# Performance work log

Measured on AMD Instinct MI355X. Metric: run time of the kernel, lower is better.

The kernel has to match this reference:

```python
import jax, jax.numpy as jnp
import numpy as np

DIM = 1024
HEADS = 16
DIM_HEAD = DIM // HEADS
SCALE = DIM_HEAD ** -0.5
LN_EPS = 1e-5


def setup_inputs() -> dict:
    key = jax.random.key(0)
    ks = jax.random.split(key, 10)
    b, n, m = 2, 2048, 2048
    s = 0.02
    return {
        "x": jax.random.normal(ks[0], (b, n, DIM), jnp.float32),
        "context": jax.random.normal(ks[1], (b, m, DIM), jnp.float32),
        "alibi": jax.random.normal(ks[2], (HEADS, n, m), jnp.float32),
        "Wq": jax.random.normal(ks[3], (DIM, DIM), jnp.float32) * s,
        "Wk": jax.random.normal(ks[4], (DIM, DIM), jnp.float32) * s,
        "Wv": jax.random.normal(ks[5], (DIM, DIM), jnp.float32) * s,
        "Wo": jax.random.normal(ks[6], (DIM, DIM), jnp.float32) * s,
        "bo": jnp.zeros((DIM,), jnp.float32),
        "ln_w": jnp.ones((DIM,), jnp.float32),
        "ln_b": jnp.zeros((DIM,), jnp.float32),
    }


def _layernorm(t, w, b):
    mu = jnp.mean(t, axis=-1, keepdims=True)
    var = jnp.var(t, axis=-1, keepdims=True)
    return (t - mu) * jax.lax.rsqrt(var + LN_EPS) * w + b


def reference(x, context, alibi, Wq, Wk, Wv, Wo, bo, ln_w, ln_b):
    xn = _layernorm(x, ln_w, ln_b)
    cn = _layernorm(context, ln_w, ln_b)
    # torch Linear: y = x @ W.T
    q = xn @ Wq.T
    k = cn @ Wk.T
    v = cn @ Wv.T
    b, n, _ = q.shape
    m = k.shape[1]
    # b n (h d) -> b h n d
    q = q.reshape(b, n, HEADS, DIM_HEAD).transpose(0, 2, 1, 3)
    k = k.reshape(b, m, HEADS, DIM_HEAD).transpose(0, 2, 1, 3)
    v = v.reshape(b, m, HEADS, DIM_HEAD).transpose(0, 2, 1, 3)
    scores = jnp.einsum("bhid,bhjd->bhij", q, k) * SCALE + alibi
    attn = jax.nn.softmax(scores, axis=-1)
    out = jnp.einsum("bhij,bhjd->bhid", attn, v)
    out = out.transpose(0, 2, 1, 3).reshape(b, n, HEADS * DIM_HEAD)
    return out @ Wo.T + bo
```

## Files before the change

kernel.cpp:

```cpp
#include <hip/hip_runtime.h>
#include <stdint.h>

#define DIM 1024
#define HEADS 16
#define DHEAD 64
#define LN_EPS 1e-5f
#define SCALE 0.125f
#define LOG2E 1.44269504089f
#define SMAX 4.0f

typedef _Float16 h8 __attribute__((ext_vector_type(8)));
typedef _Float16 h4 __attribute__((ext_vector_type(4)));
typedef _Float16 h2 __attribute__((ext_vector_type(2)));
typedef float f32x4 __attribute__((ext_vector_type(4)));

typedef __attribute__((address_space(1))) void* as1p;
typedef __attribute__((address_space(3))) void* as3p;

__device__ __forceinline__ void gl_lds16(const void* g, void* l) {
  __builtin_amdgcn_global_load_lds((as1p)g, (as3p)l, 16, 0, 0);
}

__device__ __forceinline__ float wave_sum(float v) {
#pragma unroll
  for (int o = 32; o > 0; o >>= 1) v += __shfl_xor(v, o, 64);
  return v;
}

__global__ __launch_bounds__(256) void cast4_kernel(const float* __restrict__ W0,
                                                    const float* __restrict__ W1,
                                                    const float* __restrict__ W2,
                                                    const float* __restrict__ W3,
                                                    _Float16* __restrict__ dst) {
  int gi = blockIdx.x * 256 + threadIdx.x;
  int wsel = gi >> 18;
  int li = gi & 0x3FFFF;
  const float* s = W0;
  if (wsel == 1) s = W1;
  else if (wsel == 2) s = W2;
  else if (wsel == 3) s = W3;
  float4 f = ((const float4*)s)[li];
  h4 o;
  o[0] = (_Float16)f.x; o[1] = (_Float16)f.y;
  o[2] = (_Float16)f.z; o[3] = (_Float16)f.w;
  ((h4*)dst)[gi] = o;
}

__global__ __launch_bounds__(256) void ln_f16(const float* __restrict__ x,
                                              const float* __restrict__ context,
                                              _Float16* __restrict__ out,
                                              const float* __restrict__ w,
                                              const float* __restrict__ b) {
  int row = blockIdx.x;
  const float* src = (row < 4096) ? x : context;
  int srow = row & 4095;
  const float4* rp = (const float4*)(src + (size_t)srow * DIM);
  float4 v = rp[threadIdx.x];
  float s = v.x + v.y + v.z + v.w;
  float ss = fmaf(v.x, v.x, fmaf(v.y, v.y, fmaf(v.z, v.z, v.w * v.w)));
  s = wave_sum(s);
  ss = wave_sum(ss);
  __shared__ float red[8];
  int wid = threadIdx.x >> 6, lane = threadIdx.x & 63;
  if (lane == 0) { red[wid] = s; red[4 + wid] = ss; }
  __syncthreads();
  s = red[0] + red[1] + red[2] + red[3];
  ss = red[4] + red[5] + red[6] + red[7];
  float mu = s * (1.0f / DIM);
  float var = ss * (1.0f / DIM) - mu * mu;
  float inv = rsqrtf(var + LN_EPS);
  float4 wv = ((const float4*)w)[threadIdx.x];
  float4 bv = ((const float4*)b)[threadIdx.x];
  h4 o;
  o[0] = (_Float16)((v.x - mu) * inv * wv.x + bv.x);
  o[1] = (_Float16)((v.y - mu) * inv * wv.y + bv.y);
  o[2] = (_Float16)((v.z - mu) * inv * wv.z + bv.z);
  o[3] = (_Float16)((v.w - mu) * inv * wv.w + bv.w);
  *(h4*)(out + (size_t)row * DIM + 4 * threadIdx.x) = o;
}

template <int OUT_MODE>
__device__ __forceinline__ void gemm_core128(const _Float16* __restrict__ A,
                                             const _Float16* __restrict__ W,
                                             void* __restrict__ C,
                                             const float* __restrict__ bias,
                                             int rowBase, int colBase) {
  __shared__ _Float16 As[128 * 64];
  __shared__ _Float16 Bs[128 * 64];
  int tid = threadIdx.x;
  int w = tid >> 6, lane = tid & 63;
  int quad = lane >> 4, l15 = lane & 15;
  int wr = w >> 1, wc = w & 1;
  f32x4 acc[4][4] = {};

  for (int k0 = 0; k0 < DIM; k0 += 64) {
#pragma unroll
    for (int l = 0; l < 4; l++) {
      int id = l * 256 + tid;
      int row = id & 127, c = id >> 7;
      gl_lds16(A + (size_t)(rowBase + row) * DIM + k0 + c * 8,
               &As[(l * 256 + w * 64) * 8]);
    }
#pragma unroll
    for (int l = 0; l < 4; l++) {
      int id = l * 256 + tid;
      int row = id & 127, c = id >> 7;
      gl_lds16(W + (size_t)(colBase + row) * DIM + k0 + c * 8,
               &Bs[(l * 256 + w * 64) * 8]);
    }
    __syncthreads();

    h8 af[2][4], bf[2][4];
#pragma unroll
    for (int ks = 0; ks < 2; ks++) {
#pragma unroll
      for (int mg = 0; mg < 4; mg++)
        af[ks][mg] = *(const h8*)&As[((ks * 4 + quad) * 128 + wr * 64 + mg * 16 + l15) * 8];
#pragma unroll
      for (int ng = 0; ng < 4; ng++)
        bf[ks][ng] = *(const h8*)&Bs[((ks * 4 + quad) * 128 + wc * 64 + ng * 16 + l15) * 8];
    }
#pragma unroll
    for (int mg = 0; mg < 4; mg++)
#pragma unroll
      for (int ng = 0; ng < 4; ng++)
#pragma unroll
        for (int ks = 0; ks < 2; ks++)
          acc[mg][ng] = __builtin_amdgcn_mfma_f32_16x16x32_f16(af[ks][mg], bf[ks][ng], acc[mg][ng], 0, 0, 0);
    __syncthreads();
  }

#pragma unroll
  for (int mg = 0; mg < 4; mg++)
#pragma unroll
    for (int ng = 0; ng < 4; ng++) {
      int ccol = colBase + wc * 64 + ng * 16 + l15;
      float bv = (OUT_MODE == 1) ? bias[ccol] : 0.f;
#pragma unroll
      for (int r = 0; r < 4; r++) {
        int crow = rowBase + wr * 64 + mg * 16 + quad * 4 + r;
        if (OUT_MODE == 0)
          ((_Float16*)C)[(size_t)crow * DIM + ccol] = (_Float16)acc[mg][ng][r];
        else
          ((float*)C)[(size_t)crow * DIM + ccol] = acc[mg][ng][r] + bv;
      }
    }
}

__global__ __launch_bounds__(256) void gemm_out(const _Float16* __restrict__ A,
                                                const _Float16* __restrict__ W,
                                                float* __restrict__ C,
                                                const float* __restrict__ bias) {
  gemm_core128<1>(A, W, C, bias, blockIdx.y * 128, blockIdx.x * 128);
}


#define G256_BAR __builtin_amdgcn_s_barrier()
#define G256_WV4 asm volatile("s_waitcnt vmcnt(4)" ::: "memory")
#define G256_WL0 asm volatile("s_waitcnt lgkmcnt(0)" ::: "memory")

#define G256_STG(matIsB, b, h, t)                                              \
  do {                                                                         \
    const _Float16* _src = (matIsB) ? Wbase : Abase;                           \
    int _slot = (matIsB) * 4 + (b) * 2 + (h);                                  \
    int _k0 = ((t) & 15) * 64;                                                 \
    gl_lds16(_src + (size_t)(h) * 128 * DIM + _k0 + sc * 8,                    \
             &lds[_slot * 8192 + (sc * 128 + rh64) * 8]);                      \
    gl_lds16(_src + (size_t)(h) * 128 * DIM + _k0 + (sc + 4) * 8,              \
             &lds[_slot * 8192 + ((sc + 4) * 128 + rh64) * 8]);                \
  } while (0)

#define G256_LDA(dst, b, mh)                                                   \
  do {                                                                         \
    _Pragma("unroll") for (int ks = 0; ks < 2; ks++)                           \
        _Pragma("unroll") for (int m = 0; m < 4; m++)                          \
            dst[ks][m] = *(const h8*)&lds[((b) * 2 + wr) * 8192 +              \
                ((ks * 4 + quad) * 128 + (mh) * 64 + m * 16 + l15) * 8];       \
  } while (0)

#define G256_LDB(dst, b, nh)                                                   \
  do {                                                                         \
    _Pragma("unroll") for (int ks = 0; ks < 2; ks++)                           \
        _Pragma("unroll") for (int n = 0; n < 2; n++)                          \
            dst[ks][n] = *(const h8*)&lds[(4 + (b) * 2 + (wc >> 1)) * 8192 +   \
                ((ks * 4 + quad) * 128 + (wc & 1) * 64 +                       \
                 ((nh) * 2 + n) * 16 + l15) * 8];                              \
  } while (0)

#define G256_MM(a_, b_, mh, nh)                                                \
  do {                                                                         \
    __builtin_amdgcn_s_setprio(1);                                             \
    _Pragma("unroll") for (int m = 0; m < 4; m++)                              \
        _Pragma("unroll") for (int n = 0; n < 2; n++)                          \
            _Pragma("unroll") for (int ks = 0; ks < 2; ks++)                   \
                acc[(mh) * 4 + m][(nh) * 2 + n] =                              \
                    __builtin_amdgcn_mfma_f32_16x16x32_f16(                    \
                        a_[ks][m], b_[ks][n], acc[(mh) * 4 + m][(nh) * 2 + n], \
                        0, 0, 0);                                              \
    __builtin_amdgcn_s_setprio(0);                                             \
  } while (0)

__global__ __launch_bounds__(512, 2) void gemm_qkv256(
    const _Float16* __restrict__ xnh, const _Float16* __restrict__ cnh,
    const _Float16* __restrict__ wq, const _Float16* __restrict__ wk,
    const _Float16* __restrict__ wv, _Float16* __restrict__ qo,
    _Float16* __restrict__ ko, _Float16* __restrict__ vo) {
  int z = blockIdx.z;
  const _Float16* A = (z == 0) ? xnh : cnh;
  const _Float16* W = (z == 0) ? wq : (z == 1) ? wk : wv;
  _Float16* C = (z == 0) ? qo : (z == 1) ? ko : vo;
  int rowBase = blockIdx.y * 256, colBase = blockIdx.x * 256;

  __shared__ __align__(16) _Float16 lds[8 * 8192];
  int tid = threadIdx.x;
  int w = tid >> 6, lane = tid & 63;
  int quad = lane >> 4, l15 = lane & 15;
  int wr = w >> 2, wc = w & 3;

  int sc = w >> 1;
  int rh64 = (w & 1) * 64;
  const _Float16* Abase = A + (size_t)(rowBase + rh64 + lane) * DIM;
  const _Float16* Wbase = W + (size_t)(colBase + rh64 + lane) * DIM;

  f32x4 acc[8][4] = {};
  h8 af[2][4], bf0[2][2], bf1[2][2];

  G256_STG(1, 0, 0, 0);
  G256_STG(1, 0, 1, 0);
  G256_STG(0, 0, 0, 0);
  G256_STG(0, 0, 1, 0);
  G256_STG(1, 1, 0, 1);
  G256_STG(1, 1, 1, 1);
  G256_WV4;
  G256_BAR;

  for (int i = 0; i < 8; i++) {
    int t1 = 2 * i + 1, t2 = 2 * i + 2, t3 = 2 * i + 3;
    G256_LDA(af, 0, 0);
    G256_LDB(bf0, 0, 0);
    G256_STG(0, 1, 0, t1);
    G256_BAR; G256_WL0;
    G256_MM(af, bf0, 0, 0);
    G256_BAR;
    G256_LDB(bf1, 0, 1);
    G256_STG(0, 1, 1, t1);
    G256_BAR; G256_WL0;
    G256_MM(af, bf1, 0, 1);
    G256_BAR;
    G256_LDA(af, 0, 1);
    G256_STG(1, 0, 0, t2);
    G256_BAR; G256_WL0;
    G256_MM(af, bf1, 1, 1);
    G256_BAR;
    G256_STG(1, 0, 1, t2);
    G256_BAR;
    G256_MM(af, bf0, 1, 0);
    G256_WV4;
    G256_BAR;
    G256_LDA(af, 1, 0);
    G256_LDB(bf0, 1, 0);
    G256_STG(0, 0, 0, t2);
    G256_BAR; G256_WL0;
    G256_MM(af, bf0, 0, 0);
    G256_BAR;
    G256_LDB(bf1, 1, 1);
    G256_STG(0, 0, 1, t2);
    G256_BAR; G256_WL0;
    G256_MM(af, bf1, 0, 1);
    G256_BAR;
    G256_LDA(af, 1, 1);
    G256_STG(1, 1, 0, t3);
    G256_BAR; G256_WL0;
    G256_MM(af, bf1, 1, 1);
    G256_BAR;
    G256_STG(1, 1, 1, t3);
    G256_BAR;
    G256_MM(af, bf0, 1, 0);
    G256_WV4;
    G256_BAR;
  }

#pragma unroll
  for (int m8 = 0; m8 < 8; m8++)
#pragma unroll
    for (int n4 = 0; n4 < 4; n4++) {
      int ccol = colBase + wc * 64 + n4 * 16 + l15;
#pragma unroll
      for (int r = 0; r < 4; r++) {
        int crow = rowBase + wr * 128 + m8 * 16 + quad * 4 + r;
        C[(size_t)crow * DIM + ccol] = (_Float16)acc[m8][n4][r];
      }
    }
}

__global__ __launch_bounds__(512) void attn_mfma(const _Float16* __restrict__ q,
                                                 const _Float16* __restrict__ k,
                                                 const _Float16* __restrict__ v,
                                                 const float* __restrict__ alibi,
                                                 _Float16* __restrict__ out) {
  __shared__ _Float16 Ks[2][2][64 * 64];
  __shared__ _Float16 Vt[2][2][64][72];
  __shared__ _Float16 Ps[2][8][16][72];

  int tid = threadIdx.x;
  int w = tid >> 6, lane = tid & 63;
  int quad = lane >> 4, l15 = lane & 15;
  int qbase = blockIdx.x * 128;
  int h = blockIdx.y;

  const _Float16 qs = (_Float16)(SCALE * LOG2E);
  h8 qf[2][2];
#pragma unroll
  for (int bi = 0; bi < 2; bi++) {
    const _Float16* qp = q + (size_t)(bi * 2048 + qbase + w * 16 + l15) * DIM + h * DHEAD;
    qf[bi][0] = *(const h8*)(qp + quad * 8) * qs;
    qf[bi][1] = *(const h8*)(qp + 32 + quad * 8) * qs;
  }

  h8 ones;
#pragma unroll
  for (int i = 0; i < 8; i++) ones[i] = (_Float16)1.0f;

  const float NEG_M2 = -SMAX * LOG2E;
  f32x4 l_acc[2] = {};
  f32x4 o_acc[2][4] = {};

  const float* arow_base = alibi + (size_t)h * 2048 * 2048 +
                           (size_t)(qbase + w * 16 + quad * 4) * 2048;

  int vbi = tid >> 8, vtt = tid & 255, vm = vtt & 15, vdg = vtt >> 4;

  float av[4][4];
#pragma unroll
  for (int r = 0; r < 4; r++)
#pragma unroll
    for (int ng = 0; ng < 4; ng++)
      av[r][ng] = arow_base[(size_t)r * 2048 + ng * 16 + l15];

#pragma unroll
  for (int l = 0; l < 2; l++) {
    int idx = w * 2 + l, sbi = idx >> 3, c = idx & 7;
    gl_lds16(k + (size_t)(sbi * 2048 + lane) * DIM + h * DHEAD + c * 8,
             &Ks[sbi][0][(c * 64) * 8]);
  }
  {
    const _Float16* vs = v + (size_t)(vbi * 2048 + vm) * DIM + h * DHEAD + vdg * 4;
    h4 a0 = *(const h4*)(vs);
    h4 a1 = *(const h4*)(vs + 16 * DIM);
    h4 a2 = *(const h4*)(vs + 32 * DIM);
    h4 a3 = *(const h4*)(vs + 48 * DIM);
#pragma unroll
    for (int i = 0; i < 4; i++) {
      h4 pk; pk[0] = a0[i]; pk[1] = a1[i]; pk[2] = a2[i]; pk[3] = a3[i];
      *(h4*)&Vt[vbi][0][vdg * 4 + i][4 * vm] = pk;
    }
  }
  __syncthreads();

  for (int t = 0; t < 32; t++) {
    int buf = t & 1;
    float avn[4][4];
    if (t + 1 < 32) {
      int kb1 = (t + 1) * 64;
#pragma unroll
      for (int l = 0; l < 2; l++) {
        int idx = w * 2 + l, sbi = idx >> 3, c = idx & 7;
        gl_lds16(k + (size_t)(sbi * 2048 + kb1 + lane) * DIM + h * DHEAD + c * 8,
                 &Ks[sbi][buf ^ 1][(c * 64) * 8]);
      }
      const _Float16* vs = v + (size_t)(vbi * 2048 + kb1 + vm) * DIM + h * DHEAD + vdg * 4;
      h4 a0 = *(const h4*)(vs);
      h4 a1 = *(const h4*)(vs + 16 * DIM);
      h4 a2 = *(const h4*)(vs + 32 * DIM);
      h4 a3 = *(const h4*)(vs + 48 * DIM);
#pragma unroll
      for (int i = 0; i < 4; i++) {
        h4 pk; pk[0] = a0[i]; pk[1] = a1[i]; pk[2] = a2[i]; pk[3] = a3[i];
        *(h4*)&Vt[vbi][buf ^ 1][vdg * 4 + i][4 * vm] = pk;
      }
#pragma unroll
      for (int r = 0; r < 4; r++)
#pragma unroll
        for (int ng = 0; ng < 4; ng++)
          avn[r][ng] = arow_base[(size_t)r * 2048 + kb1 + ng * 16 + l15];
    }

#pragma unroll
    for (int bi = 0; bi < 2; bi++) {
      f32x4 s_acc[4];
#pragma unroll
      for (int ng = 0; ng < 4; ng++) {
        s_acc[ng][0] = NEG_M2; s_acc[ng][1] = NEG_M2;
        s_acc[ng][2] = NEG_M2; s_acc[ng][3] = NEG_M2;
      }
#pragma unroll
      for (int ng = 0; ng < 4; ng++)
#pragma unroll
        for (int ks = 0; ks < 2; ks++) {
          h8 bfr = *(const h8*)&Ks[bi][buf][((ks * 4 + quad) * 64 + ng * 16 + l15) * 8];
          s_acc[ng] = __builtin_amdgcn_mfma_f32_16x16x32_f16(qf[bi][ks], bfr, s_acc[ng], 0, 0, 0);
        }

#pragma unroll
      for (int r = 0; r < 4; r++) {
        h4 pk;
#pragma unroll
        for (int ng = 0; ng < 4; ng++)
          pk[ng] = (_Float16)exp2f(fmaf(av[r][ng], LOG2E, s_acc[ng][r]));
        *(h4*)&Ps[bi][w][quad * 4 + r][4 * l15] = pk;
      }

      h8 pf[2];
      pf[0] = *(const h8*)&Ps[bi][w][l15][quad * 8];
      pf[1] = *(const h8*)&Ps[bi][w][l15][32 + quad * 8];
      l_acc[bi] = __builtin_amdgcn_mfma_f32_16x16x32_f16(pf[0], ones, l_acc[bi], 0, 0, 0);
      l_acc[bi] = __builtin_amdgcn_mfma_f32_16x16x32_f16(pf[1], ones, l_acc[bi], 0, 0, 0);
#pragma unroll
      for (int ngd = 0; ngd < 4; ngd++)
#pragma unroll
        for (int ks = 0; ks < 2; ks++) {
          h8 vf = *(const h8*)&Vt[bi][buf][ngd * 16 + l15][ks * 32 + quad * 8];
          o_acc[bi][ngd] = __builtin_amdgcn_mfma_f32_16x16x32_f16(pf[ks], vf, o_acc[bi][ngd], 0, 0, 0);
        }
    }

#pragma unroll
    for (int r = 0; r < 4; r++)
#pragma unroll
      for (int ng = 0; ng < 4; ng++) av[r][ng] = avn[r][ng];

    __syncthreads();
  }

#pragma unroll
  for (int bi = 0; bi < 2; bi++)
#pragma unroll
    for (int ngd = 0; ngd < 4; ngd++)
#pragma unroll
      for (int r = 0; r < 4; r++) {
        int iq = qbase + w * 16 + quad * 4 + r;
        out[(size_t)(bi * 2048 + iq) * DIM + h * DHEAD + ngd * 16 + l15] =
            (_Float16)(o_acc[bi][ngd][r] / l_acc[bi][r]);
      }
}

extern "C" void kernel_launch(void* const* d_in, const int* in_sizes, int n_in,
                              void* d_out, int out_size, void* d_ws, size_t ws_size,
                              hipStream_t stream) {
  const float* x = (const float*)d_in[0];
  const float* context = (const float*)d_in[1];
  const float* alibi = (const float*)d_in[2];
  const float* Wq = (const float*)d_in[3];
  const float* Wk = (const float*)d_in[4];
  const float* Wv = (const float*)d_in[5];
  const float* Wo = (const float*)d_in[6];
  const float* bo = (const float*)d_in[7];
  const float* ln_w = (const float*)d_in[8];
  const float* ln_b = (const float*)d_in[9];
  float* out = (float*)d_out;

  const size_t WSZ = (size_t)DIM * DIM;
  const size_t MSZ = (size_t)4096 * DIM;
  _Float16* ws16 = (_Float16*)d_ws;
  _Float16* wq_h = ws16;
  _Float16* wk_h = wq_h + WSZ;
  _Float16* wv_h = wk_h + WSZ;
  _Float16* wo_h = wv_h + WSZ;
  _Float16* xnh = wo_h + WSZ;
  _Float16* cnh = xnh + MSZ;
  _Float16* qh = cnh + MSZ;
  _Float16* kh = qh + MSZ;
  _Float16* vh = kh + MSZ;
  _Float16* aoh = vh + MSZ;

  cast4_kernel<<<4096, 256, 0, stream>>>(Wq, Wk, Wv, Wo, wq_h);
  ln_f16<<<8192, 256, 0, stream>>>(x, context, xnh, ln_w, ln_b);

  dim3 gqkv(4, 16, 3);
  gemm_qkv256<<<gqkv, 512, 0, stream>>>(xnh, cnh, wq_h, wk_h, wv_h, qh, kh, vh);

  dim3 ag(16, HEADS);
  attn_mfma<<<ag, 512, 0, stream>>>(qh, kh, vh, alibi, aoh);

  dim3 go(8, 32);
  gemm_out<<<go, 256, 0, stream>>>(aoh, wo_h, out, bo);
}
```

Baseline: 528.3 us.

## Remap block indices for XCD-local L2 reuse and fuse cast with layernorm

Block indices in the QKV GEMM, attention and output GEMM are remapped so that blocks sharing the same A rows or the same attention head land on the same XCD. Consecutive blocks are assumed to be dispatched round-robin across the 8 XCDs, and the remap is meant to improve L2 hit rates for K/V and A tiles. The weight cast kernel and the layernorm kernel are also merged into one launch to remove a kernel launch gap. The remap depends on the assumed dispatch order, and the fused kernel has blocks of uneven work.

```diff
diff --git a/kernel.cpp b/kernel.cpp
--- a/kernel.cpp
+++ b/kernel.cpp
@@ -27,31 +27,30 @@
   return v;
 }
 
-__global__ __launch_bounds__(256) void cast4_kernel(const float* __restrict__ W0,
-                                                    const float* __restrict__ W1,
-                                                    const float* __restrict__ W2,
-                                                    const float* __restrict__ W3,
-                                                    _Float16* __restrict__ dst) {
-  int gi = blockIdx.x * 256 + threadIdx.x;
-  int wsel = gi >> 18;
-  int li = gi & 0x3FFFF;
-  const float* s = W0;
-  if (wsel == 1) s = W1;
-  else if (wsel == 2) s = W2;
-  else if (wsel == 3) s = W3;
-  float4 f = ((const float4*)s)[li];
-  h4 o;
-  o[0] = (_Float16)f.x; o[1] = (_Float16)f.y;
-  o[2] = (_Float16)f.z; o[3] = (_Float16)f.w;
-  ((h4*)dst)[gi] = o;
-}
-
-__global__ __launch_bounds__(256) void ln_f16(const float* __restrict__ x,
-                                              const float* __restrict__ context,
-                                              _Float16* __restrict__ out,
-                                              const float* __restrict__ w,
-                                              const float* __restrict__ b) {
-  int row = blockIdx.x;
+__global__ __launch_bounds__(256) void castln_fused(
+    const float* __restrict__ W0, const float* __restrict__ W1,
+    const float* __restrict__ W2, const float* __restrict__ W3,
+    _Float16* __restrict__ wdst,
+    const float* __restrict__ x, const float* __restrict__ context,
+    _Float16* __restrict__ lnout,
+    const float* __restrict__ w, const float* __restrict__ b) {
+  __shared__ float red[8];
+  if (blockIdx.x < 4096) {
+    int gi = blockIdx.x * 256 + threadIdx.x;
+    int wsel = gi >> 18;
+    int li = gi & 0x3FFFF;
+    const float* s = W0;
+    if (wsel == 1) s = W1;
+    else if (wsel == 2) s = W2;
+    else if (wsel == 3) s = W3;
+    float4 f = ((const float4*)s)[li];
+    h4 o;
+    o[0] = (_Float16)f.x; o[1] = (_Float16)f.y;
+    o[2] = (_Float16)f.z; o[3] = (_Float16)f.w;
+    ((h4*)wdst)[gi] = o;
+    return;
+  }
+  int row = blockIdx.x - 4096;
   const float* src = (row < 4096) ? x : context;
   int srow = row & 4095;
   const float4* rp = (const float4*)(src + (size_t)srow * DIM);
@@ -60,7 +59,6 @@
   float ss = fmaf(v.x, v.x, fmaf(v.y, v.y, fmaf(v.z, v.z, v.w * v.w)));
   s = wave_sum(s);
   ss = wave_sum(ss);
-  __shared__ float red[8];
   int wid = threadIdx.x >> 6, lane = threadIdx.x & 63;
   if (lane == 0) { red[wid] = s; red[4 + wid] = ss; }
   __syncthreads();
@@ -76,7 +74,7 @@
   o[1] = (_Float16)((v.y - mu) * inv * wv.y + bv.y);
   o[2] = (_Float16)((v.z - mu) * inv * wv.z + bv.z);
   o[3] = (_Float16)((v.w - mu) * inv * wv.w + bv.w);
-  *(h4*)(out + (size_t)row * DIM + 4 * threadIdx.x) = o;
+  *(h4*)(lnout + (size_t)row * DIM + 4 * threadIdx.x) = o;
 }
 
 template <int OUT_MODE>
@@ -151,7 +149,11 @@
                                                 const _Float16* __restrict__ W,
                                                 float* __restrict__ C,
                                                 const float* __restrict__ bias) {
-  gemm_core128<1>(A, W, C, bias, blockIdx.y * 128, blockIdx.x * 128);
+  int L = blockIdx.x + 8 * blockIdx.y;
+  int xcd = L & 7, j = L >> 3;
+  int nbx = j >> 2;
+  int nby = xcd * 4 + (j & 3);
+  gemm_core128<1>(A, W, C, bias, nby * 128, nbx * 128);
 }
 
 
@@ -209,7 +211,11 @@
   const _Float16* A = (z == 0) ? xnh : cnh;
   const _Float16* W = (z == 0) ? wq : (z == 1) ? wk : wv;
   _Float16* C = (z == 0) ? qo : (z == 1) ? ko : vo;
-  int rowBase = blockIdx.y * 256, colBase = blockIdx.x * 256;
+  int L = blockIdx.x + 4 * blockIdx.y;
+  int xcd = L & 7, j = L >> 3;
+  int nbx = j & 3;
+  int nby = xcd * 2 + (j >> 2);
+  int rowBase = nby * 256, colBase = nbx * 256;
 
   __shared__ __align__(16) _Float16 lds[8 * 8192];
   int tid = threadIdx.x;
@@ -305,8 +311,10 @@
   int tid = threadIdx.x;
   int w = tid >> 6, lane = tid & 63;
   int quad = lane >> 4, l15 = lane & 15;
-  int qbase = blockIdx.x * 128;
-  int h = blockIdx.y;
+  int L = blockIdx.x + 16 * blockIdx.y;
+  int xcd = L & 7, j = L >> 3;
+  int h = xcd * 2 + (j >> 4);
+  int qbase = (j & 15) * 128;
 
   const _Float16 qs = (_Float16)(SCALE * LOG2E);
   h8 qf[2][2];
@@ -473,8 +481,8 @@
   _Float16* vh = kh + MSZ;
   _Float16* aoh = vh + MSZ;
 
-  cast4_kernel<<<4096, 256, 0, stream>>>(Wq, Wk, Wv, Wo, wq_h);
-  ln_f16<<<8192, 256, 0, stream>>>(x, context, xnh, ln_w, ln_b);
+  castln_fused<<<12288, 256, 0, stream>>>(Wq, Wk, Wv, Wo, wq_h,
+                                          x, context, xnh, ln_w, ln_b);
 
   dim3 gqkv(4, 16, 3);
   gemm_qkv256<<<gqkv, 512, 0, stream>>>(xnh, cnh, wq_h, wk_h, wv_h, qh, kh, vh);
```

New measurement: 522.9 us. About the same (-1.0%).
